# Optimization experiments

Measured on AMD Instinct MI355X. Metric: run time of the kernel, lower is better.

## Reference

```python
import jax, jax.numpy as jnp
import numpy as np

S, B, I, H, L, O = 2048, 64, 64, 128, 2, 1


def _lstm_dir(xs, w_ih, w_hh, b, reverse):
    # xs: (S, B, in); w_ih: (4H, in); w_hh: (4H, H); b: (4H,) = b_ih + b_hh
    # PyTorch gate order: i, f, g, o
    gx = jnp.einsum('sbi,gi->sbg', xs, w_ih) + b  # precompute input gates once
    h0 = jnp.zeros((xs.shape[1], w_hh.shape[1]), xs.dtype)
    c0 = jnp.zeros_like(h0)

    def step(carry, g_t):
        h, c = carry
        g = g_t + h @ w_hh.T
        i, f, gg, o = jnp.split(g, 4, axis=-1)
        i = jax.nn.sigmoid(i)
        f = jax.nn.sigmoid(f)
        gg = jnp.tanh(gg)
        o = jax.nn.sigmoid(o)
        c = f * c + i * gg
        h = o * jnp.tanh(c)
        return (h, c), h

    _, hs = jax.lax.scan(step, (h0, c0), gx, reverse=reverse)
    return hs  # (S, B, H), time-aligned for both directions (PyTorch semantics)


def _bilstm(x, layers):
    out = x
    for (wif, whf, bf, wir, whr, br) in layers:
        hf = _lstm_dir(out, wif, whf, bf, reverse=False)
        hb = _lstm_dir(out, wir, whr, br, reverse=True)
        out = jnp.concatenate([hf, hb], axis=-1)  # (S, B, 2H)
    return out


def setup_inputs() -> dict:
    key = jax.random.key(0)
    ks = jax.random.split(key, 16)
    sc = 1.0 / np.sqrt(H)
    u = lambda k, shp: jax.random.uniform(k, shp, jnp.float32, -sc, sc)
    inp = {
        'x': jax.random.normal(ks[0], (S, B, I), jnp.float32),
        # layer 0 (input size I)
        'w_ih_f0': u(ks[1], (4 * H, I)), 'w_hh_f0': u(ks[2], (4 * H, H)), 'b_f0': u(ks[3], (4 * H,)),
        'w_ih_r0': u(ks[4], (4 * H, I)), 'w_hh_r0': u(ks[5], (4 * H, H)), 'b_r0': u(ks[6], (4 * H,)),
        # layer 1 (input size 2H)
        'w_ih_f1': u(ks[7], (4 * H, 2 * H)), 'w_hh_f1': u(ks[8], (4 * H, H)), 'b_f1': u(ks[9], (4 * H,)),
        'w_ih_r1': u(ks[10], (4 * H, 2 * H)), 'w_hh_r1': u(ks[11], (4 * H, H)), 'b_r1': u(ks[12], (4 * H,)),
        # final linear: (O, 2H), (O,)
        'w_out': u(ks[13], (O, 2 * H)), 'b_out': u(ks[14], (O,)),
    }
    return inp


def reference(x, w_ih_f0, w_hh_f0, b_f0, w_ih_r0, w_hh_r0, b_r0,
              w_ih_f1, w_hh_f1, b_f1, w_ih_r1, w_hh_r1, b_r1, w_out, b_out):
    layers = [
        (w_ih_f0, w_hh_f0, b_f0, w_ih_r0, w_hh_r0, b_r0),
        (w_ih_f1, w_hh_f1, b_f1, w_ih_r1, w_hh_r1, b_r1),
    ]
    h = _bilstm(x, layers)                      # (S, B, 2H)
    y = jnp.einsum('sbh,oh->sbo', h, w_out) + b_out  # linear over flattened (s*b, h)
    return y
```

## Files before the change

kernel.cpp:

```cpp
#include <hip/hip_runtime.h>
#include <hip/hip_bf16.h>

#define SEQ 2048
#define NB  64

typedef _Float16 f16x8 __attribute__((ext_vector_type(8)));
typedef _Float16 f16x4 __attribute__((ext_vector_type(4)));
typedef float    f32x4 __attribute__((ext_vector_type(4)));

__device__ __forceinline__ float fast_sigmoid(float x) {
    float e = __builtin_amdgcn_exp2f(-1.4426950408889634f * x);
    return __builtin_amdgcn_rcpf(1.f + e);
}
__device__ __forceinline__ float fast_tanh(float x) {
    float e = __builtin_amdgcn_exp2f(2.8853900817779268f * x);
    return fmaf(-2.f, __builtin_amdgcn_rcpf(1.f + e), 1.f);
}

__device__ __forceinline__ void split8(const float* p4, f16x8& hi, f16x8& lo) {
    float4 a0 = *(const float4*)p4, a1 = *(const float4*)(p4 + 4);
    float av[8] = {a0.x,a0.y,a0.z,a0.w,a1.x,a1.y,a1.z,a1.w};
    #pragma unroll
    for (int e = 0; e < 8; ++e) {
        _Float16 h = (_Float16)av[e];
        hi[e] = h; lo[e] = (_Float16)(av[e] - (float)h);
    }
}


template<int PHASE>
__device__ __forceinline__ void rec_body(
    const float* __restrict__ gx,
    const float* __restrict__ Whf, const float* __restrict__ Whr,
    _Float16* __restrict__ o1, _Float16* __restrict__ o2,
    float* __restrict__ state, int tq0, int steps, int first,
    int bg, int dir)
{
    __builtin_amdgcn_s_setprio(2);
    const float* Wh = dir ? Whr : Whf;
    const int tid  = threadIdx.x;
    const int w    = tid >> 6;
    const int lane = tid & 63;
    const int col  = lane & 15;
    const int kg   = lane >> 4;
    const int kidx = 16*w + col;

    f16x8 Bhi[4][4], Blo[4][4];
    #pragma unroll
    for (int T = 0; T < 4; ++T) {
        const float* wr = Wh + (size_t)((8*T + w)*16 + col) * 128;
        #pragma unroll
        for (int ks = 0; ks < 4; ++ks)
            split8(wr + ks*32 + kg*8, Bhi[T][ks], Blo[T][ks]);
    }

    __shared__ f16x8 HhiA[256], HloA[256], HhiB[256], HloB[256];

    float cr[4], hr[4];
    float* stbase = state + ((size_t)dir*4 + bg) * 4096;
    #pragma unroll
    for (int r = 0; r < 4; ++r) {
        const int m = kg*4 + r;
        float hv = first ? 0.f : stbase[m*128 + kidx];
        float cv = first ? 0.f : stbase[2048 + m*128 + kidx];
        hr[r] = hv; cr[r] = cv;
        _Float16 hhi = (_Float16)hv;
        _Float16 hlo = (_Float16)(hv - (float)hhi);
        const int el = m*128 + (((kidx>>3) ^ m) & 15)*8 + (kidx & 7);
        ((_Float16*)HhiA)[el] = hhi;
        ((_Float16*)HloA)[el] = hlo;
    }
    __syncthreads();

    const float* gxp = gx + (size_t)(dir*4 + bg)*8192 + (size_t)lane*4;

    f32x4 gA[4], gB[4];
    #pragma unroll
    for (int T = 0; T < 4; ++T) {
        gA[T] = *(const f32x4*)(gxp + (8*T + w)*256);
        gB[T] = *(const f32x4*)(gxp + (8*T + w)*256 + 65536);
    }

    auto rec_step = [&](f32x4 (&G)[4], f16x8 (&RHI)[256], f16x8 (&RLO)[256],
                        f16x8 (&WHI)[256], f16x8 (&WLO)[256], int STEP) {
        f16x8 Ah[4], Al[4];
        #pragma unroll
        for (int ks = 0; ks < 4; ++ks) {
            const int u = col*16 + ((ks*4 + kg) ^ col);
            Ah[ks] = RHI[u];
            Al[ks] = RLO[u];
        }
        f32x4 acc0 = G[0], acc1 = G[1], acc2 = G[2], acc3 = G[3];
        const int ps = (STEP + 2 < steps) ? (STEP + 2) : (steps - 1);
        #pragma unroll
        for (int T = 0; T < 4; ++T)
            G[T] = *(const f32x4*)(gxp + (8*T + w)*256 + (size_t)ps*65536);
        #pragma unroll
        for (int ks = 0; ks < 4; ++ks) {
            acc0 = __builtin_amdgcn_mfma_f32_16x16x32_f16(Ah[ks], Bhi[0][ks], acc0, 0,0,0);
            acc0 = __builtin_amdgcn_mfma_f32_16x16x32_f16(Al[ks], Bhi[0][ks], acc0, 0,0,0);
            acc0 = __builtin_amdgcn_mfma_f32_16x16x32_f16(Ah[ks], Blo[0][ks], acc0, 0,0,0);
            acc1 = __builtin_amdgcn_mfma_f32_16x16x32_f16(Ah[ks], Bhi[1][ks], acc1, 0,0,0);
            acc1 = __builtin_amdgcn_mfma_f32_16x16x32_f16(Al[ks], Bhi[1][ks], acc1, 0,0,0);
            acc1 = __builtin_amdgcn_mfma_f32_16x16x32_f16(Ah[ks], Blo[1][ks], acc1, 0,0,0);
            acc2 = __builtin_amdgcn_mfma_f32_16x16x32_f16(Ah[ks], Bhi[2][ks], acc2, 0,0,0);
            acc2 = __builtin_amdgcn_mfma_f32_16x16x32_f16(Al[ks], Bhi[2][ks], acc2, 0,0,0);
            acc2 = __builtin_amdgcn_mfma_f32_16x16x32_f16(Ah[ks], Blo[2][ks], acc2, 0,0,0);
            acc3 = __builtin_amdgcn_mfma_f32_16x16x32_f16(Ah[ks], Bhi[3][ks], acc3, 0,0,0);
            acc3 = __builtin_amdgcn_mfma_f32_16x16x32_f16(Al[ks], Bhi[3][ks], acc3, 0,0,0);
            acc3 = __builtin_amdgcn_mfma_f32_16x16x32_f16(Ah[ks], Blo[3][ks], acc3, 0,0,0);
        }
        const int t = dir ? (SEQ-1 - tq0 - STEP) : (tq0 + STEP);
        #pragma unroll
        for (int r = 0; r < 4; ++r) {
            float iv = fast_sigmoid(acc0[r]);
            float fv = fast_sigmoid(acc1[r]);
            float gv = fast_tanh(acc2[r]);
            float ov = fast_sigmoid(acc3[r]);
            float cv = fmaf(fv, cr[r], iv * gv);
            cr[r] = cv;
            float hv = ov * fast_tanh(cv);
            hr[r] = hv;
            _Float16 hhi = (_Float16)hv;
            _Float16 hlo = (_Float16)(hv - (float)hhi);
            const int m = kg*4 + r;
            const int el = m*128 + (((kidx>>3) ^ m) & 15)*8 + (kidx & 7);
            ((_Float16*)WHI)[el] = hhi;
            ((_Float16*)WLO)[el] = hlo;
            const size_t oi = ((size_t)t*NB + (bg*16 + m))*256 + dir*128 + kidx;
            o1[oi] = hhi;
            if constexpr (PHASE == 0) o2[oi] = hlo;
        }
        asm volatile("s_waitcnt lgkmcnt(0)" ::: "memory");
        __builtin_amdgcn_s_barrier();
        asm volatile("" ::: "memory");
    };

    for (int step = 0; step < steps; step += 2) {
        rec_step(gA, HhiA, HloA, HhiB, HloB, step);
        rec_step(gB, HhiB, HloB, HhiA, HloA, step + 1);
    }

    #pragma unroll
    for (int r = 0; r < 4; ++r) {
        const int m = kg*4 + r;
        stbase[m*128 + kidx] = hr[r];
        stbase[2048 + m*128 + kidx] = cr[r];
    }
    __builtin_amdgcn_s_setprio(0);
}

template<int PHASE>
__global__ __launch_bounds__(512, 1) void megastep(
    const void* __restrict__ Agm, const _Float16* __restrict__ AloG,
    const float* __restrict__ WgF, const float* __restrict__ WgR,
    const float* __restrict__ bF, const float* __restrict__ bR,
    float* __restrict__ gxW,
    const float* __restrict__ gxR,
    const float* __restrict__ Whf, const float* __restrict__ Whr,
    _Float16* __restrict__ o1, _Float16* __restrict__ o2,
    float* __restrict__ state,
    int nrec, int tq0r, int steps, int first,
    int tq0g)
{
    const int bid = blockIdx.x;
    if (bid < nrec) {
        rec_body<PHASE>(gxR, Whf, Whr, o1, o2, state, tq0r, steps, first,
                        bid & 3, bid >> 2);
        return;
    }
    const int g    = bid - nrec;
    const int nblk = g & 7;
    const int rr   = g >> 3;
    const int half = steps >> 1;
    const int spair = rr % half;
    const int dir   = rr / half;
    const int tid  = threadIdx.x;
    const int lane = tid & 63;
    const int w8   = tid >> 6;
    const int s    = spair*2 + (w8 >> 2);
    const int wave = w8 & 3;
    const int t    = dir ? (SEQ - 1 - tq0g - s) : (tq0g + s);
    const float* W      = dir ? WgR : WgF;
    const float* bias   = dir ? bR  : bF;
    const int col = lane & 15, kg = lane >> 4;

    if constexpr (PHASE == 0) {
        const float* x = (const float*)Agm;
        const int n0 = nblk * 64;
        f32x4 acc[4] = {{0,0,0,0},{0,0,0,0},{0,0,0,0},{0,0,0,0}};
        #pragma unroll
        for (int ks = 0; ks < 2; ++ks) {
            f16x8 ahi, alo;
            split8(x + ((size_t)t*NB + wave*16 + col) * 64 + ks*32 + kg*8, ahi, alo);
            #pragma unroll
            for (int nt = 0; nt < 4; ++nt) {
                f16x8 bhi, blo;
                split8(W + (size_t)(n0 + nt*16 + col) * 64 + ks*32 + kg*8, bhi, blo);
                acc[nt] = __builtin_amdgcn_mfma_f32_16x16x32_f16(ahi, bhi, acc[nt], 0,0,0);
                acc[nt] = __builtin_amdgcn_mfma_f32_16x16x32_f16(ahi, blo, acc[nt], 0,0,0);
                acc[nt] = __builtin_amdgcn_mfma_f32_16x16x32_f16(alo, bhi, acc[nt], 0,0,0);
            }
        }
        #pragma unroll
        for (int nt = 0; nt < 4; ++nt) {
            const int n = n0 + nt*16 + col;
            const float bv = bias[n];
            f32x4 v = {acc[nt][0]+bv, acc[nt][1]+bv, acc[nt][2]+bv, acc[nt][3]+bv};
            size_t fi = (size_t)s*65536 + (size_t)(dir*4 + wave)*8192
                      + (size_t)(nblk*4 + nt)*256 + lane*4;
            *(f32x4*)(gxW + fi) = v;
        }
    } else {
        const _Float16* Ahi = (const _Float16*)Agm;
        const int wm = wave >> 1, wn = wave & 1;
        const int n0 = nblk * 64 + wn * 32;
        f32x4 acc[2][2] = {{{0,0,0,0},{0,0,0,0}},{{0,0,0,0},{0,0,0,0}}};
        #pragma unroll
        for (int ks = 0; ks < 8; ++ks) {
            f16x8 ahi[2], alo[2];
            #pragma unroll
            for (int mt = 0; mt < 2; ++mt) {
                const size_t arow = (size_t)t*NB + wm*32 + mt*16 + col;
                ahi[mt] = *(const f16x8*)(Ahi  + arow*256 + ks*32 + kg*8);
                alo[mt] = *(const f16x8*)(AloG + arow*256 + ks*32 + kg*8);
            }
            #pragma unroll
            for (int nt = 0; nt < 2; ++nt) {
                f16x8 bhi, blo;
                split8(W + (size_t)(n0 + nt*16 + col) * 256 + ks*32 + kg*8, bhi, blo);
                #pragma unroll
                for (int mt = 0; mt < 2; ++mt) {
                    acc[mt][nt] = __builtin_amdgcn_mfma_f32_16x16x32_f16(ahi[mt], bhi, acc[mt][nt], 0,0,0);
                    acc[mt][nt] = __builtin_amdgcn_mfma_f32_16x16x32_f16(ahi[mt], blo, acc[mt][nt], 0,0,0);
                    acc[mt][nt] = __builtin_amdgcn_mfma_f32_16x16x32_f16(alo[mt], bhi, acc[mt][nt], 0,0,0);
                }
            }
        }
        #pragma unroll
        for (int mt = 0; mt < 2; ++mt)
            #pragma unroll
            for (int nt = 0; nt < 2; ++nt) {
                const int n = n0 + nt*16 + col;
                const float bv = bias[n];
                f32x4 v = {acc[mt][nt][0]+bv, acc[mt][nt][1]+bv,
                           acc[mt][nt][2]+bv, acc[mt][nt][3]+bv};
                size_t fi = (size_t)s*65536 + (size_t)(dir*4 + (wm*2+mt))*8192
                          + (size_t)(nblk*4 + wn*2 + nt)*256 + lane*4;
                *(f32x4*)(gxW + fi) = v;
            }
    }
}

__global__ __launch_bounds__(256) void final_lin(
    const _Float16* __restrict__ out1,
    const float* __restrict__ wout, const float* __restrict__ bout,
    float* __restrict__ y)
{
    const int lane = threadIdx.x & 63;
    const int wave = threadIdx.x >> 6;
    const int row  = blockIdx.x * 4 + wave;
    f16x4 u = *(const f16x4*)(out1 + (size_t)row*256 + lane*4);
    float4 wv = *(const float4*)(wout + lane*4);
    float s = (float)u[0]*wv.x + (float)u[1]*wv.y + (float)u[2]*wv.z + (float)u[3]*wv.w;
    #pragma unroll
    for (int off = 32; off > 0; off >>= 1) s += __shfl_down(s, off, 64);
    if (lane == 0) y[row] = s + bout[0];
}

extern "C" void kernel_launch(void* const* d_in, const int* in_sizes, int n_in,
                              void* d_out, int out_size, void* d_ws, size_t ws_size,
                              hipStream_t stream) {
    const float* x      = (const float*)d_in[0];
    const float* wih_f0 = (const float*)d_in[1];
    const float* whh_f0 = (const float*)d_in[2];
    const float* b_f0   = (const float*)d_in[3];
    const float* wih_r0 = (const float*)d_in[4];
    const float* whh_r0 = (const float*)d_in[5];
    const float* b_r0   = (const float*)d_in[6];
    const float* wih_f1 = (const float*)d_in[7];
    const float* whh_f1 = (const float*)d_in[8];
    const float* b_f1   = (const float*)d_in[9];
    const float* wih_r1 = (const float*)d_in[10];
    const float* whh_r1 = (const float*)d_in[11];
    const float* b_r1   = (const float*)d_in[12];
    const float* w_out  = (const float*)d_in[13];
    const float* b_out  = (const float*)d_in[14];

    const size_t hB      = (size_t)SEQ*NB*256*2;
    const size_t gxStepB = 65536ull*4;

    const int cand[5] = {256, 128, 64, 32, 16};
    int Tc = 16;
    for (int i = 0; i < 5; ++i)
        if (3*hB + 2*(size_t)cand[i]*gxStepB <= ws_size) { Tc = cand[i]; break; }
    const int nq = SEQ / Tc;

    char* p = (char*)d_ws;
    _Float16* h0hi = (_Float16*)p; p += hB;
    _Float16* h0lo = (_Float16*)p; p += hB;
    _Float16* out1 = (_Float16*)p; p += hB;
    float*    gx0  = (float*)p;    p += (size_t)Tc*gxStepB;
    float*    gx1  = (float*)p;
    float*    state = (float*)d_out;

    const int ngemm = 8 * Tc;
    float* gxb[2] = {gx0, gx1};

    megastep<0><<<ngemm, 512, 0, stream>>>(
        x, nullptr, wih_f0, wih_r0, b_f0, b_r0,
        gxb[0], nullptr, nullptr, nullptr, nullptr, nullptr, nullptr,
        0, 0, Tc, 0, 0);
    for (int q = 0; q < nq; ++q) {
        const int nxt = (q + 1 < nq);
        megastep<0><<<8 + (nxt ? ngemm : 0), 512, 0, stream>>>(
            x, nullptr, wih_f0, wih_r0, b_f0, b_r0,
            gxb[(q+1)&1], gxb[q&1], whh_f0, whh_r0, h0hi, h0lo, state,
            8, q*Tc, Tc, q==0, (q+1)*Tc);
    }
    megastep<1><<<ngemm, 512, 0, stream>>>(
        h0hi, h0lo, wih_f1, wih_r1, b_f1, b_r1,
        gxb[0], nullptr, nullptr, nullptr, nullptr, nullptr, nullptr,
        0, 0, Tc, 0, 0);
    for (int q = 0; q < nq; ++q) {
        const int nxt = (q + 1 < nq);
        megastep<1><<<8 + (nxt ? ngemm : 0), 512, 0, stream>>>(
            h0hi, h0lo, wih_f1, wih_r1, b_f1, b_r1,
            gxb[(q+1)&1], gxb[q&1], whh_f1, whh_r1, out1, nullptr, state,
            8, q*Tc, Tc, q==0, (q+1)*Tc);
    }
    final_lin<<<SEQ*NB/4, 256, 0, stream>>>(out1, w_out, b_out, (float*)d_out);
}
```

Measured before the change: 5.652 ms.

## Split recurrent gate work across 16 waves with producer/consumer gate roles

Recurrent blocks now use 1024 threads: each wave computes two gate tiles instead of four, which halves the MFMA chain per wave on the serial critical path. Role-1 waves compute the g and o activations and pass them through shared memory, and role-0 waves finish the cell update. The cost is an extra barrier per step, added LDS traffic, and more threads contending per CU. The input-gate GEMM blocks are also reshaped to 1024 threads covering four timesteps each, with half as many blocks.

```diff
diff --git a/kernel.cpp b/kernel.cpp
--- a/kernel.cpp
+++ b/kernel.cpp
@@ -7,6 +7,7 @@
 typedef _Float16 f16x8 __attribute__((ext_vector_type(8)));
 typedef _Float16 f16x4 __attribute__((ext_vector_type(4)));
 typedef float    f32x4 __attribute__((ext_vector_type(4)));
+typedef float    f32x2 __attribute__((ext_vector_type(2)));
 
 __device__ __forceinline__ float fast_sigmoid(float x) {
     float e = __builtin_amdgcn_exp2f(-1.4426950408889634f * x);
@@ -43,97 +44,114 @@
     const int lane = tid & 63;
     const int col  = lane & 15;
     const int kg   = lane >> 4;
-    const int kidx = 16*w + col;
-
-    f16x8 Bhi[4][4], Blo[4][4];
+    const int cg   = w & 7;
+    const int role = w >> 3;
+    const int kidx = 16*cg + col;
+    const int gtA  = (2*role)*8 + cg;
+    const int gtB  = (2*role+1)*8 + cg;
+
+    f16x8 BAh[4], BAl[4], BBh[4], BBl[4];
     #pragma unroll
-    for (int T = 0; T < 4; ++T) {
-        const float* wr = Wh + (size_t)((8*T + w)*16 + col) * 128;
-        #pragma unroll
-        for (int ks = 0; ks < 4; ++ks)
-            split8(wr + ks*32 + kg*8, Bhi[T][ks], Blo[T][ks]);
+    for (int ks = 0; ks < 4; ++ks) {
+        split8(Wh + (size_t)(gtA*16 + col)*128 + ks*32 + kg*8, BAh[ks], BAl[ks]);
+        split8(Wh + (size_t)(gtB*16 + col)*128 + ks*32 + kg*8, BBh[ks], BBl[ks]);
     }
 
     __shared__ f16x8 HhiA[256], HloA[256], HhiB[256], HloB[256];
-
-    float cr[4], hr[4];
-    float* stbase = state + ((size_t)dir*4 + bg) * 4096;
+    __shared__ float GO[4096];
+
+    int goff[4], hel[4];
     #pragma unroll
     for (int r = 0; r < 4; ++r) {
         const int m = kg*4 + r;
-        float hv = first ? 0.f : stbase[m*128 + kidx];
-        float cv = first ? 0.f : stbase[2048 + m*128 + kidx];
-        hr[r] = hv; cr[r] = cv;
-        _Float16 hhi = (_Float16)hv;
-        _Float16 hlo = (_Float16)(hv - (float)hhi);
-        const int el = m*128 + (((kidx>>3) ^ m) & 15)*8 + (kidx & 7);
-        ((_Float16*)HhiA)[el] = hhi;
-        ((_Float16*)HloA)[el] = hlo;
+        goff[r] = (kidx*16 + (m ^ col)) * 2;
+        hel[r]  = m*128 + (((kidx>>3) ^ m) & 15)*8 + (kidx & 7);
+    }
+
+    float cr[4] = {0,0,0,0}, hr[4] = {0,0,0,0};
+    float* stbase = state + ((size_t)dir*4 + bg) * 4096;
+    if (role == 0) {
+        #pragma unroll
+        for (int r = 0; r < 4; ++r) {
+            const int m = kg*4 + r;
+            float hv = first ? 0.f : stbase[m*128 + kidx];
+            float cv = first ? 0.f : stbase[2048 + m*128 + kidx];
+            hr[r] = hv; cr[r] = cv;
+            _Float16 hhi = (_Float16)hv;
+            _Float16 hlo = (_Float16)(hv - (float)hhi);
+            ((_Float16*)HhiA)[hel[r]] = hhi;
+            ((_Float16*)HloA)[hel[r]] = hlo;
+        }
     }
     __syncthreads();
 
     const float* gxp = gx + (size_t)(dir*4 + bg)*8192 + (size_t)lane*4;
 
-    f32x4 gA[4], gB[4];
-    #pragma unroll
-    for (int T = 0; T < 4; ++T) {
-        gA[T] = *(const f32x4*)(gxp + (8*T + w)*256);
-        gB[T] = *(const f32x4*)(gxp + (8*T + w)*256 + 65536);
-    }
-
-    auto rec_step = [&](f32x4 (&G)[4], f16x8 (&RHI)[256], f16x8 (&RLO)[256],
+    f32x4 gA[2], gB[2];
+    gA[0] = *(const f32x4*)(gxp + gtA*256);
+    gA[1] = *(const f32x4*)(gxp + gtB*256);
+    gB[0] = *(const f32x4*)(gxp + gtA*256 + 65536);
+    gB[1] = *(const f32x4*)(gxp + gtB*256 + 65536);
+
+    auto rec_step = [&](f32x4 (&G)[2], f16x8 (&RHI)[256], f16x8 (&RLO)[256],
                         f16x8 (&WHI)[256], f16x8 (&WLO)[256], int STEP) {
-        f16x8 Ah[4], Al[4];
+        f32x4 accA = G[0], accB = G[1];
+        const int ps = (STEP + 2 < steps) ? (STEP + 2) : (steps - 1);
+        G[0] = *(const f32x4*)(gxp + gtA*256 + (size_t)ps*65536);
+        G[1] = *(const f32x4*)(gxp + gtB*256 + (size_t)ps*65536);
         #pragma unroll
         for (int ks = 0; ks < 4; ++ks) {
             const int u = col*16 + ((ks*4 + kg) ^ col);
-            Ah[ks] = RHI[u];
-            Al[ks] = RLO[u];
-        }
-        f32x4 acc0 = G[0], acc1 = G[1], acc2 = G[2], acc3 = G[3];
-        const int ps = (STEP + 2 < steps) ? (STEP + 2) : (steps - 1);
-        #pragma unroll
-        for (int T = 0; T < 4; ++T)
-            G[T] = *(const f32x4*)(gxp + (8*T + w)*256 + (size_t)ps*65536);
-        #pragma unroll
-        for (int ks = 0; ks < 4; ++ks) {
-            acc0 = __builtin_amdgcn_mfma_f32_16x16x32_f16(Ah[ks], Bhi[0][ks], acc0, 0,0,0);
-            acc0 = __builtin_amdgcn_mfma_f32_16x16x32_f16(Al[ks], Bhi[0][ks], acc0, 0,0,0);
-            acc0 = __builtin_amdgcn_mfma_f32_16x16x32_f16(Ah[ks], Blo[0][ks], acc0, 0,0,0);
-            acc1 = __builtin_amdgcn_mfma_f32_16x16x32_f16(Ah[ks], Bhi[1][ks], acc1, 0,0,0);
-            acc1 = __builtin_amdgcn_mfma_f32_16x16x32_f16(Al[ks], Bhi[1][ks], acc1, 0,0,0);
-            acc1 = __builtin_amdgcn_mfma_f32_16x16x32_f16(Ah[ks], Blo[1][ks], acc1, 0,0,0);
-            acc2 = __builtin_amdgcn_mfma_f32_16x16x32_f16(Ah[ks], Bhi[2][ks], acc2, 0,0,0);
-            acc2 = __builtin_amdgcn_mfma_f32_16x16x32_f16(Al[ks], Bhi[2][ks], acc2, 0,0,0);
-            acc2 = __builtin_amdgcn_mfma_f32_16x16x32_f16(Ah[ks], Blo[2][ks], acc2, 0,0,0);
-            acc3 = __builtin_amdgcn_mfma_f32_16x16x32_f16(Ah[ks], Bhi[3][ks], acc3, 0,0,0);
-            acc3 = __builtin_amdgcn_mfma_f32_16x16x32_f16(Al[ks], Bhi[3][ks], acc3, 0,0,0);
-            acc3 = __builtin_amdgcn_mfma_f32_16x16x32_f16(Ah[ks], Blo[3][ks], acc3, 0,0,0);
-        }
-        const int t = dir ? (SEQ-1 - tq0 - STEP) : (tq0 + STEP);
-        #pragma unroll
-        for (int r = 0; r < 4; ++r) {
-            float iv = fast_sigmoid(acc0[r]);
-            float fv = fast_sigmoid(acc1[r]);
-            float gv = fast_tanh(acc2[r]);
-            float ov = fast_sigmoid(acc3[r]);
-            float cv = fmaf(fv, cr[r], iv * gv);
-            cr[r] = cv;
-            float hv = ov * fast_tanh(cv);
-            hr[r] = hv;
-            _Float16 hhi = (_Float16)hv;
-            _Float16 hlo = (_Float16)(hv - (float)hhi);
-            const int m = kg*4 + r;
-            const int el = m*128 + (((kidx>>3) ^ m) & 15)*8 + (kidx & 7);
-            ((_Float16*)WHI)[el] = hhi;
-            ((_Float16*)WLO)[el] = hlo;
-            const size_t oi = ((size_t)t*NB + (bg*16 + m))*256 + dir*128 + kidx;
-            o1[oi] = hhi;
-            if constexpr (PHASE == 0) o2[oi] = hlo;
-        }
-        asm volatile("s_waitcnt lgkmcnt(0)" ::: "memory");
-        __builtin_amdgcn_s_barrier();
-        asm volatile("" ::: "memory");
+            f16x8 Ah = RHI[u];
+            f16x8 Al = RLO[u];
+            accA = __builtin_amdgcn_mfma_f32_16x16x32_f16(Ah, BAh[ks], accA, 0,0,0);
+            accA = __builtin_amdgcn_mfma_f32_16x16x32_f16(Al, BAh[ks], accA, 0,0,0);
+            accA = __builtin_amdgcn_mfma_f32_16x16x32_f16(Ah, BAl[ks], accA, 0,0,0);
+            accB = __builtin_amdgcn_mfma_f32_16x16x32_f16(Ah, BBh[ks], accB, 0,0,0);
+            accB = __builtin_amdgcn_mfma_f32_16x16x32_f16(Al, BBh[ks], accB, 0,0,0);
+            accB = __builtin_amdgcn_mfma_f32_16x16x32_f16(Ah, BBl[ks], accB, 0,0,0);
+        }
+        if (role == 1) {
+            #pragma unroll
+            for (int r = 0; r < 4; ++r) {
+                float gv = fast_tanh(accA[r]);
+                float ov = fast_sigmoid(accB[r]);
+                f32x2 v = {gv, ov};
+                *(f32x2*)(GO + goff[r]) = v;
+            }
+            asm volatile("s_waitcnt lgkmcnt(0)" ::: "memory");
+            __builtin_amdgcn_s_barrier();
+            asm volatile("" ::: "memory");
+            __builtin_amdgcn_s_barrier();
+            asm volatile("" ::: "memory");
+        } else {
+            asm volatile("s_waitcnt lgkmcnt(0)" ::: "memory");
+            __builtin_amdgcn_s_barrier();
+            asm volatile("" ::: "memory");
+            const int t = dir ? (SEQ-1 - tq0 - STEP) : (tq0 + STEP);
+            #pragma unroll
+            for (int r = 0; r < 4; ++r) {
+                float iv = fast_sigmoid(accA[r]);
+                float fv = fast_sigmoid(accB[r]);
+                f32x2 go2 = *(const f32x2*)(GO + goff[r]);
+                float gv = go2[0], ov = go2[1];
+                float cv = fmaf(fv, cr[r], iv * gv);
+                cr[r] = cv;
+                float hv = ov * fast_tanh(cv);
+                hr[r] = hv;
+                _Float16 hhi = (_Float16)hv;
+                _Float16 hlo = (_Float16)(hv - (float)hhi);
+                ((_Float16*)WHI)[hel[r]] = hhi;
+                ((_Float16*)WLO)[hel[r]] = hlo;
+                const int m = kg*4 + r;
+                const size_t oi = ((size_t)t*NB + (bg*16 + m))*256 + dir*128 + kidx;
+                o1[oi] = hhi;
+                if constexpr (PHASE == 0) o2[oi] = hlo;
+            }
+            asm volatile("s_waitcnt lgkmcnt(0)" ::: "memory");
+            __builtin_amdgcn_s_barrier();
+            asm volatile("" ::: "memory");
+        }
     };
 
     for (int step = 0; step < steps; step += 2) {
@@ -141,17 +159,19 @@
         rec_step(gB, HhiB, HloB, HhiA, HloA, step + 1);
     }
 
-    #pragma unroll
-    for (int r = 0; r < 4; ++r) {
-        const int m = kg*4 + r;
-        stbase[m*128 + kidx] = hr[r];
-        stbase[2048 + m*128 + kidx] = cr[r];
+    if (role == 0) {
+        #pragma unroll
+        for (int r = 0; r < 4; ++r) {
+            const int m = kg*4 + r;
+            stbase[m*128 + kidx] = hr[r];
+            stbase[2048 + m*128 + kidx] = cr[r];
+        }
     }
     __builtin_amdgcn_s_setprio(0);
 }
 
 template<int PHASE>
-__global__ __launch_bounds__(512, 1) void megastep(
+__global__ __launch_bounds__(1024, 4) void megastep(
     const void* __restrict__ Agm, const _Float16* __restrict__ AloG,
     const float* __restrict__ WgF, const float* __restrict__ WgR,
     const float* __restrict__ bF, const float* __restrict__ bR,
@@ -169,17 +189,17 @@
                         bid & 3, bid >> 2);
         return;
     }
-    const int g    = bid - nrec;
-    const int nblk = g & 7;
-    const int rr   = g >> 3;
-    const int half = steps >> 1;
-    const int spair = rr % half;
-    const int dir   = rr / half;
+    const int g      = bid - nrec;
+    const int nblk   = g & 7;
+    const int rr     = g >> 3;
+    const int squads = steps >> 2;
+    const int squad  = rr % squads;
+    const int dir    = rr / squads;
     const int tid  = threadIdx.x;
     const int lane = tid & 63;
-    const int w8   = tid >> 6;
-    const int s    = spair*2 + (w8 >> 2);
-    const int wave = w8 & 3;
+    const int w16  = tid >> 6;
+    const int s    = squad*4 + (w16 >> 2);
+    const int wave = w16 & 3;
     const int t    = dir ? (SEQ - 1 - tq0g - s) : (tq0g + s);
     const float* W      = dir ? WgR : WgF;
     const float* bias   = dir ? bR  : bF;
@@ -304,27 +324,27 @@
     float*    gx1  = (float*)p;
     float*    state = (float*)d_out;
 
-    const int ngemm = 8 * Tc;
+    const int ngemm = 4 * Tc;
     float* gxb[2] = {gx0, gx1};
 
-    megastep<0><<<ngemm, 512, 0, stream>>>(
+    megastep<0><<<ngemm, 1024, 0, stream>>>(
         x, nullptr, wih_f0, wih_r0, b_f0, b_r0,
         gxb[0], nullptr, nullptr, nullptr, nullptr, nullptr, nullptr,
         0, 0, Tc, 0, 0);
     for (int q = 0; q < nq; ++q) {
         const int nxt = (q + 1 < nq);
-        megastep<0><<<8 + (nxt ? ngemm : 0), 512, 0, stream>>>(
+        megastep<0><<<8 + (nxt ? ngemm : 0), 1024, 0, stream>>>(
             x, nullptr, wih_f0, wih_r0, b_f0, b_r0,
             gxb[(q+1)&1], gxb[q&1], whh_f0, whh_r0, h0hi, h0lo, state,
             8, q*Tc, Tc, q==0, (q+1)*Tc);
     }
-    megastep<1><<<ngemm, 512, 0, stream>>>(
+    megastep<1><<<ngemm, 1024, 0, stream>>>(
         h0hi, h0lo, wih_f1, wih_r1, b_f1, b_r1,
         gxb[0], nullptr, nullptr, nullptr, nullptr, nullptr, nullptr,
         0, 0, Tc, 0, 0);
     for (int q = 0; q < nq; ++q) {
         const int nxt = (q + 1 < nq);
-        megastep<1><<<8 + (nxt ? ngemm : 0), 512, 0, stream>>>(
+        megastep<1><<<8 + (nxt ? ngemm : 0), 1024, 0, stream>>>(
             h0hi, h0lo, wih_f1, wih_r1, b_f1, b_r1,
             gxb[(q+1)&1], gxb[q&1], whh_f1, whh_r1, out1, nullptr, state,
             8, q*Tc, Tc, q==0, (q+1)*Tc);
```

After: 8.598 ms. 1.52x slower.
